# Performance work log

Hardware: AMD Instinct MI355X
Metric: run time of the kernel (lower is better)

## Reference

```python
import jax, jax.numpy as jnp
import numpy as np

EMB = 2048
HD = 64            # head_dim
NH = 32            # n_heads
NKV = 8            # n_kv_groups
GS = NH // NKV     # group_size = 4
WIN = 128          # sliding_window
LAYER_IDX = 0      # even -> sliding-window mask active
ROPE_BASE = 10000.0
MAX_SEQ = 4096
YARN_ORIG = 1024.0
YARN_SCALE = 4.0
YARN_BETA_FAST = 32.0
YARN_BETA_SLOW = 1.0


def _rope_tables():
    # YaRN-adjusted RoPE tables, shape [MAX_SEQ, HD]
    freqs = 1.0 / ROPE_BASE ** (np.arange(0, HD, 2, dtype=np.float32) / HD)
    wave_len = 2.0 * np.pi / freqs
    low = YARN_ORIG / YARN_BETA_FAST
    high = YARN_ORIG / YARN_BETA_SLOW
    t = np.clip((wave_len - low) / (high - low), 0.0, 1.0)
    eff = freqs * (1.0 - t) + (freqs / YARN_SCALE) * t
    conc = 0.1 * np.log(YARN_SCALE) + 1.0
    ang = (np.arange(MAX_SEQ, dtype=np.float32)[:, None] * eff[None, :]) * conc
    ang = np.concatenate([ang, ang], axis=-1).astype(np.float32)
    return jnp.sin(ang), jnp.cos(ang)


def _apply_rope(x, sin, cos):
    # x: [B, H, S, D]; sin/cos: [B, S, D] -> broadcast over heads
    sin = sin[:, None, :, :]
    cos = cos[:, None, :, :]
    x1 = x[..., : HD // 2]
    x2 = x[..., HD // 2 :]
    rotated = jnp.concatenate([-x2, x1], axis=-1)
    return x * cos + rotated * sin


def setup_inputs() -> dict:
    key = jax.random.key(0)
    ks = jax.random.split(key, 8)
    B, S = 2, 2048
    s = 0.02
    x = jax.random.normal(ks[0], (B, S, EMB), dtype=jnp.float32)
    Wq = jax.random.normal(ks[1], (NH * HD, EMB), dtype=jnp.float32) * s
    Wk = jax.random.normal(ks[2], (NKV * HD, EMB), dtype=jnp.float32) * s
    Wv = jax.random.normal(ks[3], (NKV * HD, EMB), dtype=jnp.float32) * s
    Wo = jax.random.normal(ks[4], (EMB, NH * HD), dtype=jnp.float32) * s
    bq = jnp.zeros((NH * HD,), dtype=jnp.float32)
    bk = jnp.zeros((NKV * HD,), dtype=jnp.float32)
    bv = jnp.zeros((NKV * HD,), dtype=jnp.float32)
    bo = jnp.zeros((EMB,), dtype=jnp.float32)
    sinks = jax.random.normal(ks[5], (1, NH, 1, 1), dtype=jnp.float32)
    position_ids = jnp.arange(B * S, dtype=jnp.int64 if jax.config.jax_enable_x64 else jnp.int32).reshape(B, S)
    return {"x": x, "Wq": Wq, "bq": bq, "Wk": Wk, "bk": bk, "Wv": Wv, "bv": bv,
            "Wo": Wo, "bo": bo, "sinks": sinks, "position_ids": position_ids}


def reference(x, Wq, bq, Wk, bk, Wv, bv, Wo, bo, sinks, position_ids):
    B, S, _ = x.shape
    sin_t, cos_t = _rope_tables()
    sin = sin_t[position_ids]  # [B, S, HD]
    cos = cos_t[position_ids]

    Q = (x @ Wq.T + bq).reshape(B, S, NH, HD).transpose(0, 2, 1, 3)    # [B,NH,S,D]
    K = (x @ Wk.T + bk).reshape(B, S, NKV, HD).transpose(0, 2, 1, 3)   # [B,NKV,S,D]
    V = (x @ Wv.T + bv).reshape(B, S, NKV, HD).transpose(0, 2, 1, 3)

    Q = _apply_rope(Q, sin, cos)
    K = _apply_rope(K, sin, cos)

    # GQA without materializing repeated K/V: group query heads by kv group
    Qg = Q.reshape(B, NKV, GS, S, HD)
    scores = jnp.einsum('bgqsd,bgtd->bgqst', Qg, K) / np.sqrt(HD).astype(np.float32)

    i = jnp.arange(S)[:, None]
    j = jnp.arange(S)[None, :]
    allowed = (j <= i) & (j > i - WIN)
    scores = jnp.where(allowed, scores, -jnp.inf)

    # attention-sink logit prepended before softmax, then dropped
    sink = jnp.broadcast_to(sinks.reshape(1, NKV, GS, 1, 1), (B, NKV, GS, S, 1))
    full = jnp.concatenate([sink, scores], axis=-1)
    attn = jax.nn.softmax(full, axis=-1)[..., 1:]

    ctx = jnp.einsum('bgqst,bgtd->bgqsd', attn, V)
    ctx = ctx.reshape(B, NH, S, HD).transpose(0, 2, 1, 3).reshape(B, S, NH * HD)
    out = ctx @ Wo.T + bo
    return out
```

## Files before the change

### kernel.cpp

```cpp
#include <hip/hip_runtime.h>

typedef unsigned short u16;
typedef __bf16 bf16x8 __attribute__((ext_vector_type(8)));
typedef float f32x4 __attribute__((ext_vector_type(4)));
typedef unsigned short us8 __attribute__((ext_vector_type(8)));

__device__ inline u16 f2bf(float f) {
    union { float f; unsigned u; } v; v.f = f;
    unsigned r = v.u + 0x7FFFu + ((v.u >> 16) & 1u);
    return (u16)(r >> 16);
}
__device__ inline float bf2f(u16 h) {
    union { unsigned u; float f; } v; v.u = ((unsigned)h) << 16;
    return v.f;
}
__device__ inline f32x4 mfma16(bf16x8 a, bf16x8 b, f32x4 c) {
    return __builtin_amdgcn_mfma_f32_16x16x32_bf16(a, b, c, 0, 0, 0);
}
__device__ inline void gload_lds16(const u16* g, u16* l) {
    __builtin_amdgcn_global_load_lds(
        (const __attribute__((address_space(1))) void*)g,
        (__attribute__((address_space(3))) void*)l, 16, 0, 0);
}
union frag_cast { us8 u; bf16x8 b; };

__global__ __launch_bounds__(256)
void pack_all(const float* __restrict__ x,  const float* __restrict__ Wq,
              const float* __restrict__ Wk, const float* __restrict__ Wv,
              const float* __restrict__ Wo, const float* __restrict__ bq,
              const float* __restrict__ bk, const float* __restrict__ bv,
              u16* __restrict__ xb, u16* __restrict__ Wqkvb,
              u16* __restrict__ Wob, float* __restrict__ bqkv,
              float2* __restrict__ tab)
{
    int blk = blockIdx.x;
    if (blk >= 9217) {
        int idx = (blk - 9217) * 256 + threadIdx.x;
        int d = idx & 31, pos = idx >> 5;
        float ex = (float)d * (1.0f / 32.0f);
        float freq = powf(10000.0f, -ex);
        float wl = 6.2831853071795864f / freq;
        float tt = fminf(fmaxf((wl - 32.0f) * (1.0f / 992.0f), 0.0f), 1.0f);
        float eff = (freq * (1.0f - tt) + 0.25f * freq * tt) * 1.1386294361119891f;
        float ang = (float)pos * eff;
        tab[idx] = make_float2(cosf(ang), sinf(ang));
        return;
    }
    if (blk == 9216) {
        for (int k = threadIdx.x; k < 3072; k += 256) {
            float v;
            if (k < 2048) v = bq[k];
            else if (k < 2560) v = bk[k - 2048];
            else v = bv[k - 2560];
            bqkv[k] = v;
        }
        return;
    }
    const float* src; u16* dst; size_t off;
    if (blk < 4096)      { src = x;  dst = xb;                 off = (size_t)blk * 2048; }
    else if (blk < 6144) { src = Wq; dst = Wqkvb;              off = (size_t)(blk - 4096) * 2048; }
    else if (blk < 6656) { src = Wk; dst = Wqkvb + 4194304;    off = (size_t)(blk - 6144) * 2048; }
    else if (blk < 7168) { src = Wv; dst = Wqkvb + 5242880;    off = (size_t)(blk - 6656) * 2048; }
    else                 { src = Wo; dst = Wob;                off = (size_t)(blk - 7168) * 2048; }
    size_t i = off + (size_t)threadIdx.x * 8;
    float4 v0 = *(const float4*)(src + i);
    float4 v1 = *(const float4*)(src + i + 4);
    us8 w;
    w[0] = f2bf(v0.x); w[1] = f2bf(v0.y); w[2] = f2bf(v0.z); w[3] = f2bf(v0.w);
    w[4] = f2bf(v1.x); w[5] = f2bf(v1.y); w[6] = f2bf(v1.z); w[7] = f2bf(v1.w);
    *(us8*)(dst + i) = w;
}

template<int WNF, int VC1, int OUT_BF16>
__global__ __launch_bounds__(512, 2)
void gemm_dp(const u16* __restrict__ A, const u16* __restrict__ B,
             const float* __restrict__ bias, void* __restrict__ Yv,
             int M, int N, int K)
{
    constexpr int BN = 32 * WNF;
    constexpr int BSL = BN * 32;
    constexpr int ABUF = 16384;
    constexpr int BUFU = ABUF + 2 * BSL;
    __shared__ u16 lds[2 * BUFU];

    const int tid = threadIdx.x;
    const int lane = tid & 63;
    const int w = tid >> 6;
    const int wr = w >> 1, wc = w & 1;
    const int wg = blockIdx.x;
    const int swz = (wg & 7) * 32 + (wg >> 3);
    const int by = swz >> 4, bx = swz & 15;
    const long m0 = (long)by * 256;
    const long n0 = (long)bx * BN;
    const int cc = lane & 15, qq = lane >> 4;
    const int csw = (qq ^ ((cc >> 1) & 3)) << 3;

    const int sr = lane >> 2;
    const int colsw = ((lane & 3) ^ ((lane >> 3) & 3)) << 3;
    const u16* Ag = A + (m0 + sr) * (long)K + colsw;
    const u16* Bg = B + (n0 + sr) * (long)K + colsw;

    const int NT = K >> 6;

    auto STAGE0 = [&](int u) {
        u16* buf = &lds[(u & 1) * BUFU];
        const long k0 = (long)u * 64;
        gload_lds16(Ag + (size_t)(w * 16) * K + k0,        buf + (w * 16) * 32);
        gload_lds16(Ag + (size_t)(128 + w * 16) * K + k0,  buf + (128 + w * 16) * 32);
        gload_lds16(Bg + (size_t)(w * 16) * K + k0,        buf + ABUF + (w * 16) * 32);
        if (WNF == 6) {
            if (w < 4)
                gload_lds16(Bg + (size_t)(128 + w * 16) * K + k0,
                            buf + ABUF + (128 + w * 16) * 32);
            else
                gload_lds16(Bg + (size_t)((w - 4) * 16) * K + k0 + 32,
                            buf + ABUF + BSL + ((w - 4) * 16) * 32);
        }
    };
    auto STAGE1 = [&](int u) {
        u16* buf = &lds[(u & 1) * BUFU];
        const long k0 = (long)u * 64 + 32;
        gload_lds16(Ag + (size_t)(w * 16) * K + k0,        buf + 8192 + (w * 16) * 32);
        gload_lds16(Ag + (size_t)(128 + w * 16) * K + k0,  buf + 8192 + (128 + w * 16) * 32);
        if (WNF == 6)
            gload_lds16(Bg + (size_t)((w + 4) * 16) * K + k0,
                        buf + ABUF + BSL + ((w + 4) * 16) * 32);
        else
            gload_lds16(Bg + (size_t)(w * 16) * K + k0,
                        buf + ABUF + BSL + (w * 16) * 32);
    };

    f32x4 acc[4][WNF];
#pragma unroll
    for (int m = 0; m < 4; ++m)
#pragma unroll
        for (int n = 0; n < WNF; ++n) acc[m][n] = (f32x4){0.f, 0.f, 0.f, 0.f};

    STAGE0(0);
    STAGE1(0);

    for (int t = 0; t < NT; ++t) {
        const u16* buf = &lds[(t & 1) * BUFU];

        asm volatile("s_waitcnt vmcnt(3)" ::: "memory");
        __builtin_amdgcn_s_barrier();
        __builtin_amdgcn_sched_barrier(0);
        {
            const u16* Ab = buf;
            const u16* Bb = buf + ABUF;
            bf16x8 af[4], bfr[WNF];
#pragma unroll
            for (int n = 0; n < WNF; ++n)
                bfr[n] = *(const bf16x8*)&Bb[(wc * (16 * WNF) + n * 16 + cc) * 32 + csw];
#pragma unroll
            for (int m = 0; m < 4; ++m)
                af[m] = *(const bf16x8*)&Ab[(wr * 64 + m * 16 + cc) * 32 + csw];
            if (t + 1 < NT) STAGE0(t + 1);
            __builtin_amdgcn_sched_barrier(0);
            __builtin_amdgcn_s_setprio(1);
#pragma unroll
            for (int m = 0; m < 4; ++m)
#pragma unroll
                for (int n = 0; n < WNF; ++n)
                    acc[m][n] = mfma16(af[m], bfr[n], acc[m][n]);
            __builtin_amdgcn_s_setprio(0);
            __builtin_amdgcn_sched_barrier(0);
        }

        if (t + 1 < NT) {
            if (VC1 == 4) asm volatile("s_waitcnt vmcnt(4)" ::: "memory");
            else          asm volatile("s_waitcnt vmcnt(3)" ::: "memory");
        } else {
            asm volatile("s_waitcnt vmcnt(0)" ::: "memory");
        }
        __builtin_amdgcn_s_barrier();
        __builtin_amdgcn_sched_barrier(0);
        {
            const u16* Ab = buf + 8192;
            const u16* Bb = buf + ABUF + BSL;
            bf16x8 af[4], bfr[WNF];
#pragma unroll
            for (int n = 0; n < WNF; ++n)
                bfr[n] = *(const bf16x8*)&Bb[(wc * (16 * WNF) + n * 16 + cc) * 32 + csw];
#pragma unroll
            for (int m = 0; m < 4; ++m)
                af[m] = *(const bf16x8*)&Ab[(wr * 64 + m * 16 + cc) * 32 + csw];
            if (t + 1 < NT) STAGE1(t + 1);
            __builtin_amdgcn_sched_barrier(0);
            __builtin_amdgcn_s_setprio(1);
#pragma unroll
            for (int m = 0; m < 4; ++m)
#pragma unroll
                for (int n = 0; n < WNF; ++n)
                    acc[m][n] = mfma16(af[m], bfr[n], acc[m][n]);
            __builtin_amdgcn_s_setprio(0);
            __builtin_amdgcn_sched_barrier(0);
        }
    }

#pragma unroll
    for (int m = 0; m < 4; ++m) {
#pragma unroll
        for (int n = 0; n < WNF; ++n) {
            long row = m0 + wr * 64 + m * 16 + qq * 4;
            long col = n0 + wc * (16 * WNF) + n * 16 + cc;
            float bvv = bias[col];
#pragma unroll
            for (int r2 = 0; r2 < 4; ++r2) {
                float v = acc[m][n][r2] + bvv;
                if (OUT_BF16)
                    ((u16*)Yv)[(row + r2) * (long)N + col] = f2bf(v);
                else
                    ((float*)Yv)[(row + r2) * (long)N + col] = v;
            }
        }
    }
}

__global__ __launch_bounds__(256)
void v_transpose(const u16* __restrict__ Vt, u16* __restrict__ VbT)
{
    __shared__ u16 tile[64][66];
    int s0 = blockIdx.x * 64;
    int bkv = blockIdx.y;
    int b = bkv >> 3, kv = bkv & 7;
    int t = threadIdx.x;
#pragma unroll
    for (int it = 0; it < 16; ++it) {
        int idx = t + it * 256;
        int s = idx >> 6, d = idx & 63;
        tile[s][d] = Vt[((size_t)(b * 2048 + s0 + s)) * 3072 + 2560 + kv * 64 + d];
    }
    __syncthreads();
#pragma unroll
    for (int it = 0; it < 16; ++it) {
        int idx = t + it * 256;
        int d = idx >> 6, s = idx & 63;
        VbT[((size_t)(bkv * 64 + d)) * 2048 + s0 + s] = tile[s][d];
    }
}

__global__ __launch_bounds__(256, 2)
void attn_win2(const u16* __restrict__ QKVr, const u16* __restrict__ VbT,
               const float2* __restrict__ tab, const int* __restrict__ pid,
               const float* __restrict__ sinks, u16* __restrict__ Ctx)
{
    __shared__ u16 Ks[192 * 72];
    __shared__ u16 Vs[64 * 200];
    __shared__ u16 Pb[4 * 16 * 200];
    const int S = 2048;
    const int tid = threadIdx.x;
    const int lane = tid & 63;
    const int w = tid >> 6;
    const int cc = lane & 15, qq = lane >> 4;
    const int blk = blockIdx.x;
    const int qt = blk & 31;
    const int bkv = blk >> 5;
    const int b = bkv >> 3, kv = bkv & 7;
    const int q0 = qt * 64;
    const int ks0 = q0 - 128;
    const int h = kv * 4 + w;

    {
        const int kcol = 2048 + kv * 64;
#pragma unroll
        for (int it = 0; it < 3; ++it) {
            int c = tid + it * 256;
            int kk = c >> 2, dlo = (c & 3) << 3;
            int sk = ks0 + kk;
            us8 lo = {0, 0, 0, 0, 0, 0, 0, 0};
            us8 hi = {0, 0, 0, 0, 0, 0, 0, 0};
            if (sk >= 0) {
                size_t rowoff = (size_t)(b * S + sk) * 3072 + kcol;
                us8 li = *(const us8*)(QKVr + rowoff + dlo);
                us8 hiQ = *(const us8*)(QKVr + rowoff + dlo + 32);
                int pos = pid[b * S + sk];
                const float2* tp = tab + pos * 32 + dlo;
#pragma unroll
                for (int jj = 0; jj < 8; ++jj) {
                    float2 cs = tp[jj];
                    float x1 = bf2f(li[jj]), x2 = bf2f(hiQ[jj]);
                    lo[jj] = f2bf(x1 * cs.x - x2 * cs.y);
                    hi[jj] = f2bf(x2 * cs.x + x1 * cs.y);
                }
            }
            *(us8*)&Ks[kk * 72 + dlo] = lo;
            *(us8*)&Ks[kk * 72 + dlo + 32] = hi;
        }
    }
    const u16* VtBase = VbT + (size_t)bkv * 64 * S;
#pragma unroll
    for (int it = 0; it < 6; ++it) {
        int c = tid + it * 256;
        int d = c / 24, kc = c % 24;
        int kk0 = kc << 3;
        int sk = ks0 + kk0;
        us8 v = {0, 0, 0, 0, 0, 0, 0, 0};
        if (sk >= 0) v = *(const us8*)(VtBase + (size_t)d * S + sk);
        *(us8*)&Vs[d * 200 + kk0] = v;
    }
    __syncthreads();

    const float sinkv = sinks[h];
    u16* Pw = &Pb[w * 3200];

    for (int i = 0; i < 4; ++i) {
        int m = b * S + q0 + i * 16 + cc;
        const u16* Qrow = QKVr + (size_t)m * 3072 + h * 64;
        us8 qlo = *(const us8*)(Qrow + qq * 8);
        us8 qhi = *(const us8*)(Qrow + 32 + qq * 8);
        int pos = pid[m];
        const float2* tp = tab + pos * 32 + qq * 8;
        frag_cast a0, a1;
#pragma unroll
        for (int jj = 0; jj < 8; ++jj) {
            float2 cs = tp[jj];
            float x1 = bf2f(qlo[jj]), x2 = bf2f(qhi[jj]);
            a0.u[jj] = f2bf(x1 * cs.x - x2 * cs.y);
            a1.u[jj] = f2bf(x2 * cs.x + x1 * cs.y);
        }
        bf16x8 aq0 = a0.b, aq1 = a1.b;

        f32x4 sc[12];
#pragma unroll
        for (int j = 0; j < 12; j++) sc[j] = (f32x4){0.f, 0.f, 0.f, 0.f};
#pragma unroll
        for (int j = 0; j < 12; j++) {
            bf16x8 b0 = *(const bf16x8*)&Ks[(j * 16 + cc) * 72 + qq * 8];
            bf16x8 b1 = *(const bf16x8*)&Ks[(j * 16 + cc) * 72 + 32 + qq * 8];
            sc[j] = mfma16(aq0, b0, sc[j]);
            sc[j] = mfma16(aq1, b1, sc[j]);
        }

#pragma unroll
        for (int r = 0; r < 4; ++r) {
            int qi = i * 16 + qq * 4 + r;
            float sval[12];
            float mx = -3.0e38f;
#pragma unroll
            for (int j = 0; j < 12; j++) {
                int kk = j * 16 + cc;
                float s = sc[j][r] * 0.125f;
                bool ok = (kk > qi) && (kk <= qi + 128) && (ks0 + kk >= 0);
                s = ok ? s : -3.0e38f;
                sval[j] = s;
                mx = fmaxf(mx, s);
            }
#pragma unroll
            for (int off = 1; off < 16; off <<= 1) mx = fmaxf(mx, __shfl_xor(mx, off));
            mx = fmaxf(mx, sinkv);
            float sum = 0.f;
#pragma unroll
            for (int j = 0; j < 12; j++) {
                float p = __expf(sval[j] - mx);
                sval[j] = p;
                sum += p;
            }
#pragma unroll
            for (int off = 1; off < 16; off <<= 1) sum += __shfl_xor(sum, off);
            float rden = 1.0f / (sum + __expf(sinkv - mx));
#pragma unroll
            for (int j = 0; j < 12; j++)
                Pw[(qq * 4 + r) * 200 + j * 16 + cc] = f2bf(sval[j] * rden);
        }

        f32x4 o[4];
#pragma unroll
        for (int jt = 0; jt < 4; jt++) o[jt] = (f32x4){0.f, 0.f, 0.f, 0.f};
#pragma unroll
        for (int ks = 0; ks < 6; ks++) {
            bf16x8 ap = *(const bf16x8*)&Pw[cc * 200 + ks * 32 + qq * 8];
#pragma unroll
            for (int jt = 0; jt < 4; jt++) {
                bf16x8 bv = *(const bf16x8*)&Vs[(jt * 16 + cc) * 200 + ks * 32 + qq * 8];
                o[jt] = mfma16(ap, bv, o[jt]);
            }
        }
#pragma unroll
        for (int jt = 0; jt < 4; jt++) {
#pragma unroll
            for (int r = 0; r < 4; r++) {
                size_t off = ((size_t)(b * S + q0 + i * 16 + qq * 4 + r)) * 2048
                           + h * 64 + jt * 16 + cc;
                Ctx[off] = f2bf(o[jt][r]);
            }
        }
    }
}

extern "C" void kernel_launch(void* const* d_in, const int* in_sizes, int n_in,
                              void* d_out, int out_size, void* d_ws, size_t ws_size,
                              hipStream_t stream)
{
    const float* x    = (const float*)d_in[0];
    const float* Wq   = (const float*)d_in[1];
    const float* bq   = (const float*)d_in[2];
    const float* Wk   = (const float*)d_in[3];
    const float* bk   = (const float*)d_in[4];
    const float* Wv   = (const float*)d_in[5];
    const float* bv   = (const float*)d_in[6];
    const float* Wo   = (const float*)d_in[7];
    const float* bo   = (const float*)d_in[8];
    const float* sinks = (const float*)d_in[9];
    const int*   pid  = (const int*)d_in[10];
    float* out = (float*)d_out;

    char*  ws    = (char*)d_ws;
    u16*   Wqkvb = (u16*)ws;
    u16*   Wob   = (u16*)(ws + 12582912);
    u16*   xb    = (u16*)(ws + 20971520);
    u16*   Ctx   = xb;
    u16*   QKVr  = (u16*)(ws + 37748736);
    u16*   VbT   = (u16*)(ws + 62914560);
    float* bqkv  = (float*)(ws + 67108864);
    float2* tab  = (float2*)(ws + 67121152);

    pack_all<<<9729, 256, 0, stream>>>(x, Wq, Wk, Wv, Wo, bq, bk, bv,
                                       xb, Wqkvb, Wob, bqkv, tab);

    gemm_dp<6, 4, 1><<<256, 512, 0, stream>>>(xb, Wqkvb, bqkv, QKVr,
                                              4096, 3072, 2048);

    v_transpose<<<dim3(32, 16), 256, 0, stream>>>(QKVr, VbT);

    attn_win2<<<512, 256, 0, stream>>>(QKVr, VbT, tab, pid, sinks, Ctx);

    gemm_dp<4, 3, 0><<<256, 512, 0, stream>>>(Ctx, Wob, bo, out,
                                              4096, 2048, 2048);
}
```

Before: 251.1 us.

## Restructure GEMM main loop into one barrier per tile with phased LDS reads

The GEMM now issues the whole next 64-wide k-tile prefetch at once and waits for all outstanding loads with a single barrier per iteration, instead of two half-tile stages each with its own barrier. The MFMA work is split into four phases that interleave LDS fragment reads with MFMA groups, aiming to hide LDS latency and halve barrier count. The cost is a full vmcnt(0) wait each iteration, which exposes more global-load latency since the prefetch has only one tile of compute to hide behind.

```diff
diff --git a/kernel.cpp b/kernel.cpp
--- a/kernel.cpp
+++ b/kernel.cpp
@@ -71,9 +71,9 @@
     *(us8*)(dst + i) = w;
 }
 
-template<int WNF, int VC1, int OUT_BF16>
+template<int WNF, int OUT_BF16>
 __global__ __launch_bounds__(512, 2)
-void gemm_dp(const u16* __restrict__ A, const u16* __restrict__ B,
+void gemm_ph(const u16* __restrict__ A, const u16* __restrict__ B,
              const float* __restrict__ bias, void* __restrict__ Yv,
              int M, int N, int K)
 {
@@ -81,6 +81,7 @@
     constexpr int BSL = BN * 32;
     constexpr int ABUF = 16384;
     constexpr int BUFU = ABUF + 2 * BSL;
+    constexpr int NH2 = WNF / 2;
     __shared__ u16 lds[2 * BUFU];
 
     const int tid = threadIdx.x;
@@ -102,12 +103,12 @@
 
     const int NT = K >> 6;
 
-    auto STAGE0 = [&](int u) {
+    auto STAGE = [&](int u) {
         u16* buf = &lds[(u & 1) * BUFU];
         const long k0 = (long)u * 64;
-        gload_lds16(Ag + (size_t)(w * 16) * K + k0,        buf + (w * 16) * 32);
-        gload_lds16(Ag + (size_t)(128 + w * 16) * K + k0,  buf + (128 + w * 16) * 32);
-        gload_lds16(Bg + (size_t)(w * 16) * K + k0,        buf + ABUF + (w * 16) * 32);
+        gload_lds16(Ag + (size_t)(w * 16) * K + k0,       buf + (w * 16) * 32);
+        gload_lds16(Ag + (size_t)(128 + w * 16) * K + k0, buf + (128 + w * 16) * 32);
+        gload_lds16(Bg + (size_t)(w * 16) * K + k0,       buf + ABUF + (w * 16) * 32);
         if (WNF == 6) {
             if (w < 4)
                 gload_lds16(Bg + (size_t)(128 + w * 16) * K + k0,
@@ -116,17 +117,13 @@
                 gload_lds16(Bg + (size_t)((w - 4) * 16) * K + k0 + 32,
                             buf + ABUF + BSL + ((w - 4) * 16) * 32);
         }
-    };
-    auto STAGE1 = [&](int u) {
-        u16* buf = &lds[(u & 1) * BUFU];
-        const long k0 = (long)u * 64 + 32;
-        gload_lds16(Ag + (size_t)(w * 16) * K + k0,        buf + 8192 + (w * 16) * 32);
-        gload_lds16(Ag + (size_t)(128 + w * 16) * K + k0,  buf + 8192 + (128 + w * 16) * 32);
+        gload_lds16(Ag + (size_t)(w * 16) * K + k0 + 32,       buf + 8192 + (w * 16) * 32);
+        gload_lds16(Ag + (size_t)(128 + w * 16) * K + k0 + 32, buf + 8192 + (128 + w * 16) * 32);
         if (WNF == 6)
-            gload_lds16(Bg + (size_t)((w + 4) * 16) * K + k0,
+            gload_lds16(Bg + (size_t)((w + 4) * 16) * K + k0 + 32,
                         buf + ABUF + BSL + ((w + 4) * 16) * 32);
         else
-            gload_lds16(Bg + (size_t)(w * 16) * K + k0,
+            gload_lds16(Bg + (size_t)(w * 16) * K + k0 + 32,
                         buf + ABUF + BSL + (w * 16) * 32);
     };
 
@@ -136,66 +133,82 @@
 #pragma unroll
         for (int n = 0; n < WNF; ++n) acc[m][n] = (f32x4){0.f, 0.f, 0.f, 0.f};
 
-    STAGE0(0);
-    STAGE1(0);
+    STAGE(0);
 
     for (int t = 0; t < NT; ++t) {
         const u16* buf = &lds[(t & 1) * BUFU];
-
-        asm volatile("s_waitcnt vmcnt(3)" ::: "memory");
+        const u16* Ab0 = buf;
+        const u16* Ab1 = buf + 8192;
+        const u16* Bb0 = buf + ABUF;
+        const u16* Bb1 = buf + ABUF + BSL;
+
+        asm volatile("s_waitcnt vmcnt(0)" ::: "memory");
         __builtin_amdgcn_s_barrier();
         __builtin_amdgcn_sched_barrier(0);
-        {
-            const u16* Ab = buf;
-            const u16* Bb = buf + ABUF;
-            bf16x8 af[4], bfr[WNF];
-#pragma unroll
-            for (int n = 0; n < WNF; ++n)
-                bfr[n] = *(const bf16x8*)&Bb[(wc * (16 * WNF) + n * 16 + cc) * 32 + csw];
-#pragma unroll
-            for (int m = 0; m < 4; ++m)
-                af[m] = *(const bf16x8*)&Ab[(wr * 64 + m * 16 + cc) * 32 + csw];
-            if (t + 1 < NT) STAGE0(t + 1);
-            __builtin_amdgcn_sched_barrier(0);
-            __builtin_amdgcn_s_setprio(1);
-#pragma unroll
-            for (int m = 0; m < 4; ++m)
-#pragma unroll
-                for (int n = 0; n < WNF; ++n)
-                    acc[m][n] = mfma16(af[m], bfr[n], acc[m][n]);
-            __builtin_amdgcn_s_setprio(0);
-            __builtin_amdgcn_sched_barrier(0);
-        }
-
-        if (t + 1 < NT) {
-            if (VC1 == 4) asm volatile("s_waitcnt vmcnt(4)" ::: "memory");
-            else          asm volatile("s_waitcnt vmcnt(3)" ::: "memory");
-        } else {
-            asm volatile("s_waitcnt vmcnt(0)" ::: "memory");
-        }
-        __builtin_amdgcn_s_barrier();
-        __builtin_amdgcn_sched_barrier(0);
-        {
-            const u16* Ab = buf + 8192;
-            const u16* Bb = buf + ABUF + BSL;
-            bf16x8 af[4], bfr[WNF];
-#pragma unroll
-            for (int n = 0; n < WNF; ++n)
-                bfr[n] = *(const bf16x8*)&Bb[(wc * (16 * WNF) + n * 16 + cc) * 32 + csw];
-#pragma unroll
-            for (int m = 0; m < 4; ++m)
-                af[m] = *(const bf16x8*)&Ab[(wr * 64 + m * 16 + cc) * 32 + csw];
-            if (t + 1 < NT) STAGE1(t + 1);
-            __builtin_amdgcn_sched_barrier(0);
-            __builtin_amdgcn_s_setprio(1);
-#pragma unroll
-            for (int m = 0; m < 4; ++m)
-#pragma unroll
-                for (int n = 0; n < WNF; ++n)
-                    acc[m][n] = mfma16(af[m], bfr[n], acc[m][n]);
-            __builtin_amdgcn_s_setprio(0);
-            __builtin_amdgcn_sched_barrier(0);
-        }
+        if (t + 1 < NT) STAGE(t + 1);
+        __builtin_amdgcn_sched_barrier(0);
+
+        bf16x8 a0[4], a1[4], bA[NH2], bB[NH2], bC[NH2], bD[NH2];
+
+#pragma unroll
+        for (int m = 0; m < 4; ++m)
+            a0[m] = *(const bf16x8*)&Ab0[(wr * 64 + m * 16 + cc) * 32 + csw];
+#pragma unroll
+        for (int n = 0; n < NH2; ++n)
+            bA[n] = *(const bf16x8*)&Bb0[(wc * (16 * WNF) + n * 16 + cc) * 32 + csw];
+#pragma unroll
+        for (int n = 0; n < NH2; ++n)
+            bB[n] = *(const bf16x8*)&Bb0[(wc * (16 * WNF) + (NH2 + n) * 16 + cc) * 32 + csw];
+        __builtin_amdgcn_sched_barrier(0);
+
+        __builtin_amdgcn_s_setprio(1);
+#pragma unroll
+        for (int m = 0; m < 4; ++m)
+#pragma unroll
+            for (int n = 0; n < NH2; ++n)
+                acc[m][n] = mfma16(a0[m], bA[n], acc[m][n]);
+        __builtin_amdgcn_s_setprio(0);
+        __builtin_amdgcn_sched_barrier(0);
+
+#pragma unroll
+        for (int m = 0; m < 4; ++m)
+            a1[m] = *(const bf16x8*)&Ab1[(wr * 64 + m * 16 + cc) * 32 + csw];
+#pragma unroll
+        for (int n = 0; n < NH2; ++n)
+            bC[n] = *(const bf16x8*)&Bb1[(wc * (16 * WNF) + n * 16 + cc) * 32 + csw];
+        __builtin_amdgcn_sched_barrier(0);
+
+        __builtin_amdgcn_s_setprio(1);
+#pragma unroll
+        for (int m = 0; m < 4; ++m)
+#pragma unroll
+            for (int n = 0; n < NH2; ++n)
+                acc[m][NH2 + n] = mfma16(a0[m], bB[n], acc[m][NH2 + n]);
+        __builtin_amdgcn_s_setprio(0);
+        __builtin_amdgcn_sched_barrier(0);
+
+#pragma unroll
+        for (int n = 0; n < NH2; ++n)
+            bD[n] = *(const bf16x8*)&Bb1[(wc * (16 * WNF) + (NH2 + n) * 16 + cc) * 32 + csw];
+        __builtin_amdgcn_sched_barrier(0);
+
+        __builtin_amdgcn_s_setprio(1);
+#pragma unroll
+        for (int m = 0; m < 4; ++m)
+#pragma unroll
+            for (int n = 0; n < NH2; ++n)
+                acc[m][n] = mfma16(a1[m], bC[n], acc[m][n]);
+        __builtin_amdgcn_s_setprio(0);
+        __builtin_amdgcn_sched_barrier(0);
+
+        __builtin_amdgcn_s_setprio(1);
+#pragma unroll
+        for (int m = 0; m < 4; ++m)
+#pragma unroll
+            for (int n = 0; n < NH2; ++n)
+                acc[m][NH2 + n] = mfma16(a1[m], bD[n], acc[m][NH2 + n]);
+        __builtin_amdgcn_s_setprio(0);
+        __builtin_amdgcn_sched_barrier(0);
     }
 
 #pragma unroll
@@ -418,13 +431,13 @@
     pack_all<<<9729, 256, 0, stream>>>(x, Wq, Wk, Wv, Wo, bq, bk, bv,
                                        xb, Wqkvb, Wob, bqkv, tab);
 
-    gemm_dp<6, 4, 1><<<256, 512, 0, stream>>>(xb, Wqkvb, bqkv, QKVr,
-                                              4096, 3072, 2048);
+    gemm_ph<6, 1><<<256, 512, 0, stream>>>(xb, Wqkvb, bqkv, QKVr,
+                                           4096, 3072, 2048);
 
     v_transpose<<<dim3(32, 16), 256, 0, stream>>>(QKVr, VbT);
 
     attn_win2<<<512, 256, 0, stream>>>(QKVr, VbT, tab, pid, sinks, Ctx);
 
-    gemm_dp<4, 3, 0><<<256, 512, 0, stream>>>(Ctx, Wob, bo, out,
-                                              4096, 2048, 2048);
-}
+    gemm_ph<4, 0><<<256, 512, 0, stream>>>(Ctx, Wob, bo, out,
+                                           4096, 2048, 2048);
+}
```

Result: no change. 254.6 us (+1.4%).
